# Kernel optimization log

Hardware: AMD Instinct MI355X
Metric: run time of the kernel (lower is better)

## Reference

```python
import jax, jax.numpy as jnp
import numpy as np

N_NODES = 100000
N_EDGES = 2500000
IN_CH = 32
HID = 16
OUT_CH = 32


def setup_inputs() -> dict:
    key = jax.random.key(0)
    ks = jax.random.split(key, 10)
    x = jax.random.normal(ks[0], (N_NODES, IN_CH), dtype=jnp.float32)
    edge_index = jax.random.randint(ks[1], (2, N_EDGES), 0, N_NODES, dtype=jnp.int64)
    # conv1 MLP: Linear(in,16) -> ReLU -> Linear(16,out)
    W1 = jax.random.normal(ks[2], (IN_CH, HID), dtype=jnp.float32) / np.sqrt(IN_CH)
    b1 = jnp.zeros((HID,), dtype=jnp.float32)
    W2 = jax.random.normal(ks[3], (HID, OUT_CH), dtype=jnp.float32) / np.sqrt(HID)
    b2 = jnp.zeros((OUT_CH,), dtype=jnp.float32)
    # conv2 MLP: Linear(out,16) -> ReLU -> Linear(16,out)
    W3 = jax.random.normal(ks[4], (OUT_CH, HID), dtype=jnp.float32) / np.sqrt(OUT_CH)
    b3 = jnp.zeros((HID,), dtype=jnp.float32)
    W4 = jax.random.normal(ks[5], (HID, OUT_CH), dtype=jnp.float32) / np.sqrt(HID)
    b4 = jnp.zeros((OUT_CH,), dtype=jnp.float32)
    return {"x": x, "edge_index": edge_index, "W1": W1, "b1": b1, "W2": W2,
            "b2": b2, "W3": W3, "b3": b3, "W4": W4, "b4": b4}


def _gin_conv(x, src, dst, W_a, b_a, W_b, b_b):
    # GINConv (eps=0): nn((1+eps)*x + sum_{j in N(i)} x_j)
    agg = jax.ops.segment_sum(x[src], dst, num_segments=x.shape[0])  # [N, d]
    h = x + agg
    h = jnp.maximum(h @ W_a + b_a, 0.0)  # Linear -> ReLU
    return h @ W_b + b_b                 # Linear


def reference(x, edge_index, W1, b1, W2, b2, W3, b3, W4, b4):
    src, dst = edge_index[0], edge_index[1]
    h = _gin_conv(x, src, dst, W1, b1, W2, b2)
    h = jnp.maximum(h, 0.0)  # F.relu between convs
    out = _gin_conv(h, src, dst, W3, b3, W4, b4)
    return out
```

## Files before the change

### kernel.cpp

```cpp
#include <hip/hip_runtime.h>

typedef unsigned short ushort_t;
typedef unsigned int uint_t;

#define BKT_SHIFT 6
#define BKT_NODES 64
#define NBKT_MAX 1600
#define BCAP 2560
#define EPB 8192
#define HCAP 40
#define CAPP 81

__device__ __forceinline__ ushort_t f2bf(float f) {
    unsigned u = __float_as_uint(f);
    unsigned r = (u + 0x7FFFu + ((u >> 16) & 1u)) >> 16;
    return (ushort_t)r;
}
__device__ __forceinline__ float bflo(uint_t u) { return __uint_as_float(u << 16); }
__device__ __forceinline__ float bfhi(uint_t u) { return __uint_as_float(u & 0xFFFF0000u); }

__global__ __launch_bounds__(512) void scatter_lin(
    const int* __restrict__ src, const int* __restrict__ dst,
    int* __restrict__ gcnt, int* __restrict__ staged,
    const float4* __restrict__ x4, const float* __restrict__ W,
    ushort_t* __restrict__ z, int E, int SBLK, int N, int NBKT)
{
    __shared__ float sW[512];
    __shared__ int lcnt[NBKT_MAX];
    __shared__ int lbase[NBKT_MAX];
    __shared__ int lcur[NBKT_MAX];
    int t = threadIdx.x, blk = blockIdx.x;
    if (blk < SBLK) {
        for (int b = t; b < NBKT; b += 512) { lcnt[b] = 0; lcur[b] = 0; }
        __syncthreads();
        int e0 = blk * EPB;
        int rd[16], rs[16];
        #pragma unroll
        for (int i = 0; i < 16; ++i) {
            int e = e0 + i * 512 + t;
            bool ok = (e < E);
            rd[i] = ok ? dst[e] : -1;
            rs[i] = ok ? src[e] : 0;
            if (ok) atomicAdd(&lcnt[rd[i] >> BKT_SHIFT], 1);
        }
        __syncthreads();
        for (int b = t; b < NBKT; b += 512)
            lbase[b] = atomicAdd(&gcnt[b], lcnt[b]);
        __syncthreads();
        #pragma unroll
        for (int i = 0; i < 16; ++i) {
            if (rd[i] >= 0) {
                int b = rd[i] >> BKT_SHIFT;
                int r = lbase[b] + atomicAdd(&lcur[b], 1);
                if (r < BCAP)
                    staged[(size_t)b * BCAP + r] =
                        ((rd[i] & (BKT_NODES - 1)) << 24) | rs[i];
            }
        }
    } else {
        sW[t] = W[t];
        __syncthreads();
        int n = (blk - SBLK) * 512 + t;
        if (n >= N) return;
        float a[16];
        #pragma unroll
        for (int c = 0; c < 16; ++c) a[c] = 0.f;
        const float4* xr = x4 + (size_t)n * 8;
        #pragma unroll
        for (int k4 = 0; k4 < 8; ++k4) {
            float4 xv = xr[k4];
            #pragma unroll
            for (int c = 0; c < 16; ++c) {
                a[c] += xv.x * sW[(k4 * 4 + 0) * 16 + c];
                a[c] += xv.y * sW[(k4 * 4 + 1) * 16 + c];
                a[c] += xv.z * sW[(k4 * 4 + 2) * 16 + c];
                a[c] += xv.w * sW[(k4 * 4 + 3) * 16 + c];
            }
        }
        uint_t w[8];
        #pragma unroll
        for (int i2 = 0; i2 < 8; ++i2)
            w[i2] = (uint_t)f2bf(a[2 * i2]) | ((uint_t)f2bf(a[2 * i2 + 1]) << 16);
        uint4* zo = (uint4*)(z + (size_t)n * 16);
        uint4 q0; q0.x = w[0]; q0.y = w[1]; q0.z = w[2]; q0.w = w[3];
        uint4 q1; q1.x = w[4]; q1.y = w[5]; q1.z = w[6]; q1.w = w[7];
        zo[0] = q0;
        zo[1] = q1;
    }
}


template <bool CHAIN>
__global__ __launch_bounds__(256) void agg_slot_mlp(
    const ushort_t* __restrict__ zin, const int* __restrict__ staged,
    const int* __restrict__ gcnt,
    const float* __restrict__ ba,
    const float* __restrict__ Wb, const float* __restrict__ bb,
    const float* __restrict__ Wc,
    void* __restrict__ outv, int N)
{
    __shared__ float sWb[512];
    __shared__ float sWc[512];
    __shared__ float sba[16], sbb[32];
    __shared__ float sh[BKT_NODES * 17];
    __shared__ float sr[BKT_NODES * 33];
    __shared__ int cnt2[BKT_NODES * 2];
    __shared__ int slots[BKT_NODES * CAPP];

    int t = threadIdx.x;
    sWb[t] = Wb[t];  sWb[t + 256] = Wb[t + 256];
    if (CHAIN) { sWc[t] = Wc[t];  sWc[t + 256] = Wc[t + 256]; }
    if (t < 16) sba[t] = ba[t];
    if (t < 32) sbb[t] = bb[t];
    if (t < BKT_NODES * 2) cnt2[t] = 0;
    __syncthreads();

    int b = blockIdx.x;
    int m = min(gcnt[b], BCAP);
    const int* sp = staged + (size_t)b * BCAP;

    for (int i = t; i < m; i += 256) {
        int v = sp[i];
        int dl = ((unsigned)v) >> 24;
        int h = v & 1;
        int r = atomicAdd(&cnt2[dl * 2 + h], 1);
        if (r < HCAP)
            slots[dl * CAPP + h * HCAP + r] = v & 0xFFFFFF;
    }
    __syncthreads();

    int ln = t >> 2;
    int sl = t & 3;
    int n  = (b << BKT_SHIFT) + ln;
    bool act = (n < N);
    const uint2* zp = (const uint2*)zin;

    if (act) {
        uint2 us = zp[(size_t)n * 4 + sl];
        float v0 = bflo(us.x), v1 = bfhi(us.x), v2 = bflo(us.y), v3 = bfhi(us.y);
        #pragma unroll
        for (int h = 0; h < 2; ++h) {
            int kend = min(cnt2[ln * 2 + h], HCAP);
            const int* sl0 = &slots[ln * CAPP + h * HCAP];
            int k = 0;
            for (; k + 8 <= kend; k += 8) {
                int s0 = sl0[k + 0], s1 = sl0[k + 1], s2 = sl0[k + 2], s3 = sl0[k + 3];
                int s4 = sl0[k + 4], s5 = sl0[k + 5], s6 = sl0[k + 6], s7 = sl0[k + 7];
                uint2 u0 = zp[(size_t)s0 * 4 + sl];
                uint2 u1 = zp[(size_t)s1 * 4 + sl];
                uint2 u2 = zp[(size_t)s2 * 4 + sl];
                uint2 u3 = zp[(size_t)s3 * 4 + sl];
                uint2 u4 = zp[(size_t)s4 * 4 + sl];
                uint2 u5 = zp[(size_t)s5 * 4 + sl];
                uint2 u6 = zp[(size_t)s6 * 4 + sl];
                uint2 u7 = zp[(size_t)s7 * 4 + sl];
                v0 += ((bflo(u0.x) + bflo(u1.x)) + (bflo(u2.x) + bflo(u3.x)))
                    + ((bflo(u4.x) + bflo(u5.x)) + (bflo(u6.x) + bflo(u7.x)));
                v1 += ((bfhi(u0.x) + bfhi(u1.x)) + (bfhi(u2.x) + bfhi(u3.x)))
                    + ((bfhi(u4.x) + bfhi(u5.x)) + (bfhi(u6.x) + bfhi(u7.x)));
                v2 += ((bflo(u0.y) + bflo(u1.y)) + (bflo(u2.y) + bflo(u3.y)))
                    + ((bflo(u4.y) + bflo(u5.y)) + (bflo(u6.y) + bflo(u7.y)));
                v3 += ((bfhi(u0.y) + bfhi(u1.y)) + (bfhi(u2.y) + bfhi(u3.y)))
                    + ((bfhi(u4.y) + bfhi(u5.y)) + (bfhi(u6.y) + bfhi(u7.y)));
            }
            for (; k < kend; ++k) {
                uint2 u = zp[(size_t)sl0[k] * 4 + sl];
                v0 += bflo(u.x); v1 += bfhi(u.x); v2 += bflo(u.y); v3 += bfhi(u.y);
            }
        }
        int cb = sl * 4;
        sh[ln * 17 + cb + 0] = fmaxf(v0 + sba[cb + 0], 0.f);
        sh[ln * 17 + cb + 1] = fmaxf(v1 + sba[cb + 1], 0.f);
        sh[ln * 17 + cb + 2] = fmaxf(v2 + sba[cb + 2], 0.f);
        sh[ln * 17 + cb + 3] = fmaxf(v3 + sba[cb + 3], 0.f);
    }
    __syncthreads();

    if (act) {
        int c0 = sl * 8;
        float o[8];
        #pragma unroll
        for (int j = 0; j < 8; ++j) o[j] = sbb[c0 + j];
        #pragma unroll
        for (int j = 0; j < 16; ++j) {
            float hj = sh[ln * 17 + j];
            #pragma unroll
            for (int cc = 0; cc < 8; ++cc)
                o[cc] += hj * sWb[j * 32 + c0 + cc];
        }
        if (CHAIN) {
            #pragma unroll
            for (int cc = 0; cc < 8; ++cc)
                sr[ln * 33 + c0 + cc] = fmaxf(o[cc], 0.f);
        } else {
            float* op = (float*)outv + (size_t)n * 32 + c0;
            #pragma unroll
            for (int cc = 0; cc < 8; ++cc)
                __builtin_nontemporal_store(o[cc], op + cc);
        }
    }
    if (CHAIN) {
        __syncthreads();
        if (act) {
            int c0 = sl * 4;
            float a0 = 0.f, a1 = 0.f, a2 = 0.f, a3 = 0.f;
            #pragma unroll
            for (int j = 0; j < 32; ++j) {
                float rj = sr[ln * 33 + j];
                a0 += rj * sWc[j * 16 + c0 + 0];
                a1 += rj * sWc[j * 16 + c0 + 1];
                a2 += rj * sWc[j * 16 + c0 + 2];
                a3 += rj * sWc[j * 16 + c0 + 3];
            }
            uint_t p0 = (uint_t)f2bf(a0) | ((uint_t)f2bf(a1) << 16);
            uint_t p1 = (uint_t)f2bf(a2) | ((uint_t)f2bf(a3) << 16);
            uint_t* op = (uint_t*)outv + (size_t)n * 8 + sl * 2;
            op[0] = p0;
            op[1] = p1;
        }
    }
}


extern "C" void kernel_launch(void* const* d_in, const int* in_sizes, int n_in,
                              void* d_out, int out_size, void* d_ws, size_t ws_size,
                              hipStream_t stream) {
    const float* x  = (const float*)d_in[0];
    const int*   ei = (const int*)d_in[1];
    const float* W1 = (const float*)d_in[2];
    const float* b1 = (const float*)d_in[3];
    const float* W2 = (const float*)d_in[4];
    const float* b2 = (const float*)d_in[5];
    const float* W3 = (const float*)d_in[6];
    const float* b3 = (const float*)d_in[7];
    const float* W4 = (const float*)d_in[8];
    const float* b4 = (const float*)d_in[9];

    const int N = in_sizes[0] / 32;
    const int E = in_sizes[1] / 2;
    const int* src = ei;
    const int* dst = ei + E;

    const int NBKT = (N + BKT_NODES - 1) >> BKT_SHIFT;
    const int SBLK = (E + EPB - 1) / EPB;
    const int LINB = (N + 511) / 512;

    char* ws = (char*)d_ws;
    size_t o = 0;
    auto alloc = [&](size_t bytes) -> char* {
        o = (o + 255) & ~(size_t)255;
        char* r = ws + o;
        o += bytes;
        return r;
    };
    int*      gcnt   = (int*)     alloc(4 * (size_t)NBKT);
    int*      staged = (int*)     alloc(4 * (size_t)NBKT * BCAP);
    ushort_t* zb     = (ushort_t*)alloc(2 * (size_t)N * 16);
    ushort_t* z2b    = (ushort_t*)alloc(2 * (size_t)N * 16);

    (void)hipMemsetAsync(gcnt, 0, 4 * (size_t)NBKT, stream);

    scatter_lin<<<SBLK + LINB, 512, 0, stream>>>(
        src, dst, gcnt, staged, (const float4*)x, W1, zb, E, SBLK, N, NBKT);

    agg_slot_mlp<true ><<<NBKT, 256, 0, stream>>>(
        zb, staged, gcnt, b1, W2, b2, W3, z2b, N);
    agg_slot_mlp<false><<<NBKT, 256, 0, stream>>>(
        z2b, staged, gcnt, b3, W4, b4, nullptr, (float*)d_out, N);
}
```

Baseline: 180.5 us.

## Replace shared-memory MLP staging with wave shuffles and prefetch bucket loads

Removes the sh/sr shared-memory buffers and their barriers from the aggregation+MLP kernel. The per-node hidden vector is now exchanged among the four lanes of a node with __shfl_xor, and the second projection is reduced with shuffles instead of being staged in LDS. It also issues the self-feature load before the slot-bucketing loop, software-prefetches staged edges with nontemporal loads, and requests 5 blocks per CU in launch bounds. The intent is lower LDS use and fewer syncs for higher occupancy and better latency hiding, at the cost of more registers per thread and some redundant FMAs per lane.

```diff
diff --git a/kernel.cpp b/kernel.cpp
--- a/kernel.cpp
+++ b/kernel.cpp
@@ -91,7 +91,7 @@
 
 
 template <bool CHAIN>
-__global__ __launch_bounds__(256) void agg_slot_mlp(
+__global__ __launch_bounds__(256, 5) void agg_slot_mlp(
     const ushort_t* __restrict__ zin, const int* __restrict__ staged,
     const int* __restrict__ gcnt,
     const float* __restrict__ ba,
@@ -102,8 +102,6 @@
     __shared__ float sWb[512];
     __shared__ float sWc[512];
     __shared__ float sba[16], sbb[32];
-    __shared__ float sh[BKT_NODES * 17];
-    __shared__ float sr[BKT_NODES * 33];
     __shared__ int cnt2[BKT_NODES * 2];
     __shared__ int slots[BKT_NODES * CAPP];
 
@@ -119,25 +117,32 @@
     int m = min(gcnt[b], BCAP);
     const int* sp = staged + (size_t)b * BCAP;
 
-    for (int i = t; i < m; i += 256) {
-        int v = sp[i];
-        int dl = ((unsigned)v) >> 24;
-        int h = v & 1;
-        int r = atomicAdd(&cnt2[dl * 2 + h], 1);
-        if (r < HCAP)
-            slots[dl * CAPP + h * HCAP + r] = v & 0xFFFFFF;
-    }
-    __syncthreads();
-
     int ln = t >> 2;
     int sl = t & 3;
     int n  = (b << BKT_SHIFT) + ln;
     bool act = (n < N);
     const uint2* zp = (const uint2*)zin;
 
+    uint2 us = act ? zp[(size_t)n * 4 + sl] : make_uint2(0u, 0u);
+
+    {
+        int i = t;
+        int v = (i < m) ? __builtin_nontemporal_load(sp + i) : -1;
+        while (i < m) {
+            int inext = i + 256;
+            int vn = (inext < m) ? __builtin_nontemporal_load(sp + inext) : -1;
+            int dl = ((unsigned)v) >> 24;
+            int h = v & 1;
+            int r = atomicAdd(&cnt2[dl * 2 + h], 1);
+            if (r < HCAP)
+                slots[dl * CAPP + h * HCAP + r] = v & 0xFFFFFF;
+            v = vn; i = inext;
+        }
+    }
+    __syncthreads();
+
+    float acc[4] = { bflo(us.x), bfhi(us.x), bflo(us.y), bfhi(us.y) };
     if (act) {
-        uint2 us = zp[(size_t)n * 4 + sl];
-        float v0 = bflo(us.x), v1 = bfhi(us.x), v2 = bflo(us.y), v3 = bfhi(us.y);
         #pragma unroll
         for (int h = 0; h < 2; ++h) {
             int kend = min(cnt2[ln * 2 + h], HCAP);
@@ -154,69 +159,77 @@
                 uint2 u5 = zp[(size_t)s5 * 4 + sl];
                 uint2 u6 = zp[(size_t)s6 * 4 + sl];
                 uint2 u7 = zp[(size_t)s7 * 4 + sl];
-                v0 += ((bflo(u0.x) + bflo(u1.x)) + (bflo(u2.x) + bflo(u3.x)))
-                    + ((bflo(u4.x) + bflo(u5.x)) + (bflo(u6.x) + bflo(u7.x)));
-                v1 += ((bfhi(u0.x) + bfhi(u1.x)) + (bfhi(u2.x) + bfhi(u3.x)))
-                    + ((bfhi(u4.x) + bfhi(u5.x)) + (bfhi(u6.x) + bfhi(u7.x)));
-                v2 += ((bflo(u0.y) + bflo(u1.y)) + (bflo(u2.y) + bflo(u3.y)))
-                    + ((bflo(u4.y) + bflo(u5.y)) + (bflo(u6.y) + bflo(u7.y)));
-                v3 += ((bfhi(u0.y) + bfhi(u1.y)) + (bfhi(u2.y) + bfhi(u3.y)))
-                    + ((bfhi(u4.y) + bfhi(u5.y)) + (bfhi(u6.y) + bfhi(u7.y)));
+                acc[0] += ((bflo(u0.x) + bflo(u1.x)) + (bflo(u2.x) + bflo(u3.x)))
+                        + ((bflo(u4.x) + bflo(u5.x)) + (bflo(u6.x) + bflo(u7.x)));
+                acc[1] += ((bfhi(u0.x) + bfhi(u1.x)) + (bfhi(u2.x) + bfhi(u3.x)))
+                        + ((bfhi(u4.x) + bfhi(u5.x)) + (bfhi(u6.x) + bfhi(u7.x)));
+                acc[2] += ((bflo(u0.y) + bflo(u1.y)) + (bflo(u2.y) + bflo(u3.y)))
+                        + ((bflo(u4.y) + bflo(u5.y)) + (bflo(u6.y) + bflo(u7.y)));
+                acc[3] += ((bfhi(u0.y) + bfhi(u1.y)) + (bfhi(u2.y) + bfhi(u3.y)))
+                        + ((bfhi(u4.y) + bfhi(u5.y)) + (bfhi(u6.y) + bfhi(u7.y)));
             }
             for (; k < kend; ++k) {
                 uint2 u = zp[(size_t)sl0[k] * 4 + sl];
-                v0 += bflo(u.x); v1 += bfhi(u.x); v2 += bflo(u.y); v3 += bfhi(u.y);
-            }
-        }
-        int cb = sl * 4;
-        sh[ln * 17 + cb + 0] = fmaxf(v0 + sba[cb + 0], 0.f);
-        sh[ln * 17 + cb + 1] = fmaxf(v1 + sba[cb + 1], 0.f);
-        sh[ln * 17 + cb + 2] = fmaxf(v2 + sba[cb + 2], 0.f);
-        sh[ln * 17 + cb + 3] = fmaxf(v3 + sba[cb + 3], 0.f);
-    }
-    __syncthreads();
+                acc[0] += bflo(u.x); acc[1] += bfhi(u.x);
+                acc[2] += bflo(u.y); acc[3] += bfhi(u.y);
+            }
+        }
+    }
+
+    float h0[4], h1[4], h2[4], h3[4];
+    #pragma unroll
+    for (int j = 0; j < 4; ++j) h0[j] = fmaxf(acc[j] + sba[sl * 4 + j], 0.f);
+    #pragma unroll
+    for (int j = 0; j < 4; ++j) h1[j] = __shfl_xor(h0[j], 1);
+    #pragma unroll
+    for (int j = 0; j < 4; ++j) h2[j] = __shfl_xor(h0[j], 2);
+    #pragma unroll
+    for (int j = 0; j < 4; ++j) h3[j] = __shfl_xor(h1[j], 2);
+    int cb0 = sl * 4, cb1 = (sl ^ 1) * 4, cb2 = (sl ^ 2) * 4, cb3 = (sl ^ 3) * 4;
+    int ob = sl * 8;
+    float o[8];
+    #pragma unroll
+    for (int oc = 0; oc < 8; ++oc) o[oc] = sbb[ob + oc];
+    #pragma unroll
+    for (int j = 0; j < 4; ++j) {
+        #pragma unroll
+        for (int oc = 0; oc < 8; ++oc) {
+            o[oc] += h0[j] * sWb[(cb0 + j) * 32 + ob + oc];
+            o[oc] += h1[j] * sWb[(cb1 + j) * 32 + ob + oc];
+            o[oc] += h2[j] * sWb[(cb2 + j) * 32 + ob + oc];
+            o[oc] += h3[j] * sWb[(cb3 + j) * 32 + ob + oc];
+        }
+    }
 
     if (act) {
-        int c0 = sl * 8;
-        float o[8];
-        #pragma unroll
-        for (int j = 0; j < 8; ++j) o[j] = sbb[c0 + j];
-        #pragma unroll
-        for (int j = 0; j < 16; ++j) {
-            float hj = sh[ln * 17 + j];
-            #pragma unroll
-            for (int cc = 0; cc < 8; ++cc)
-                o[cc] += hj * sWb[j * 32 + c0 + cc];
-        }
         if (CHAIN) {
-            #pragma unroll
-            for (int cc = 0; cc < 8; ++cc)
-                sr[ln * 33 + c0 + cc] = fmaxf(o[cc], 0.f);
+            float p[16];
+            #pragma unroll
+            for (int zc = 0; zc < 16; ++zc) p[zc] = 0.f;
+            #pragma unroll
+            for (int i = 0; i < 8; ++i) {
+                float r = fmaxf(o[i], 0.f);
+                #pragma unroll
+                for (int zc = 0; zc < 16; ++zc)
+                    p[zc] += r * sWc[(ob + i) * 16 + zc];
+            }
+            #pragma unroll
+            for (int zc = 0; zc < 16; ++zc) p[zc] += __shfl_xor(p[zc], 1);
+            #pragma unroll
+            for (int zc = 0; zc < 16; ++zc) p[zc] += __shfl_xor(p[zc], 2);
+            float zA = (sl == 0) ? p[0]  : (sl == 1) ? p[4]  : (sl == 2) ? p[8]  : p[12];
+            float zB = (sl == 0) ? p[1]  : (sl == 1) ? p[5]  : (sl == 2) ? p[9]  : p[13];
+            float zC = (sl == 0) ? p[2]  : (sl == 1) ? p[6]  : (sl == 2) ? p[10] : p[14];
+            float zD = (sl == 0) ? p[3]  : (sl == 1) ? p[7]  : (sl == 2) ? p[11] : p[15];
+            uint2 q;
+            q.x = (uint_t)f2bf(zA) | ((uint_t)f2bf(zB) << 16);
+            q.y = (uint_t)f2bf(zC) | ((uint_t)f2bf(zD) << 16);
+            ((uint2*)outv)[(size_t)n * 4 + sl] = q;
         } else {
-            float* op = (float*)outv + (size_t)n * 32 + c0;
-            #pragma unroll
-            for (int cc = 0; cc < 8; ++cc)
-                __builtin_nontemporal_store(o[cc], op + cc);
-        }
-    }
-    if (CHAIN) {
-        __syncthreads();
-        if (act) {
-            int c0 = sl * 4;
-            float a0 = 0.f, a1 = 0.f, a2 = 0.f, a3 = 0.f;
-            #pragma unroll
-            for (int j = 0; j < 32; ++j) {
-                float rj = sr[ln * 33 + j];
-                a0 += rj * sWc[j * 16 + c0 + 0];
-                a1 += rj * sWc[j * 16 + c0 + 1];
-                a2 += rj * sWc[j * 16 + c0 + 2];
-                a3 += rj * sWc[j * 16 + c0 + 3];
-            }
-            uint_t p0 = (uint_t)f2bf(a0) | ((uint_t)f2bf(a1) << 16);
-            uint_t p1 = (uint_t)f2bf(a2) | ((uint_t)f2bf(a3) << 16);
-            uint_t* op = (uint_t*)outv + (size_t)n * 8 + sl * 2;
-            op[0] = p0;
-            op[1] = p1;
+            float* op = (float*)outv + (size_t)n * 32 + ob;
+            #pragma unroll
+            for (int oc = 0; oc < 8; ++oc)
+                __builtin_nontemporal_store(o[oc], op + oc);
         }
     }
 }
```

After: 183.8 us. About the same (+1.8%).
